# Kernel optimization log

Hardware: AMD Instinct MI355X
Metric: run time of the kernel (lower is better)

## Reference

```python
import jax, jax.numpy as jnp
import numpy as np

EMBED_DIM = 768
N_HEADS = 12
HEAD_DIM = EMBED_DIM // N_HEADS
B, T = 2, 4096


def setup_inputs() -> dict:
    key = jax.random.key(0)
    k1, k2, k3, k4, k5 = jax.random.split(key, 5)
    s = 1.0 / np.sqrt(EMBED_DIM)
    return {
        "x": jax.random.normal(k1, (B, T, EMBED_DIM), dtype=jnp.float32),
        "Wqkv": jax.random.normal(k2, (EMBED_DIM, 3 * EMBED_DIM), dtype=jnp.float32) * s,
        "bqkv": jnp.zeros((3 * EMBED_DIM,), dtype=jnp.float32),
        "Wproj": jax.random.normal(k3, (EMBED_DIM, EMBED_DIM), dtype=jnp.float32) * s,
        "bproj": jnp.zeros((EMBED_DIM,), dtype=jnp.float32),
    }


def reference(x, Wqkv, bqkv, Wproj, bproj):
    Bz, Tz, C = x.shape
    qkv = x @ Wqkv + bqkv                         # [B,T,3C]
    q, k, v = jnp.split(qkv, 3, axis=2)
    # [B,T,H,D] -> [B,H,T,D]
    def heads(t):
        return t.reshape(Bz, Tz, N_HEADS, HEAD_DIM).transpose(0, 2, 1, 3)
    q, k, v = heads(q), heads(k), heads(v)
    scale = 1.0 / np.sqrt(HEAD_DIM)
    att = jnp.einsum("bhqd,bhkd->bhqk", q, k) * scale   # [B,H,T,T]
    causal = jnp.tril(jnp.ones((Tz, Tz), dtype=bool))
    att = jnp.where(causal[None, None], att, -jnp.inf)
    att = jax.nn.softmax(att, axis=-1)
    y = jnp.einsum("bhqk,bhkd->bhqd", att, v)            # [B,H,T,D]
    y = y.transpose(0, 2, 1, 3).reshape(Bz, Tz, C)
    return y @ Wproj + bproj
```

## Files before the change

### kernel.cpp

```cpp
#include <hip/hip_runtime.h>
#include <math.h>
#include <stdint.h>

typedef __attribute__((ext_vector_type(8))) short bf16x8;
typedef __attribute__((ext_vector_type(4))) float f32x4;

__device__ __forceinline__ unsigned short f2bf(float f) {
    union { float f; unsigned u; } v; v.f = f;
    return (unsigned short)((v.u + 0x7fffu + ((v.u >> 16) & 1u)) >> 16);
}

__device__ __forceinline__ void gld_lds16(const void* g, void* l) {
    __builtin_amdgcn_global_load_lds(
        (const __attribute__((address_space(1))) unsigned*)(uintptr_t)g,
        (__attribute__((address_space(3))) unsigned*)(uintptr_t)l, 16, 0, 0);
}

__global__ void k_convert(const float* __restrict__ in, unsigned short* __restrict__ out, int n4) {
    int i = blockIdx.x * blockDim.x + threadIdx.x;
    if (i >= n4) return;
    float4 f = ((const float4*)in)[i];
    ushort4 o;
    o.x = f2bf(f.x); o.y = f2bf(f.y); o.z = f2bf(f.z); o.w = f2bf(f.w);
    ((ushort4*)out)[i] = o;
}

__global__ void k_transpose(const float* __restrict__ in, unsigned short* __restrict__ out, int R, int C) {
    __shared__ float tile[32][33];
    int c0 = blockIdx.x * 32, r0 = blockIdx.y * 32;
    int tx = threadIdx.x, ty = threadIdx.y;
#pragma unroll
    for (int i = 0; i < 4; ++i)
        tile[ty + i * 8][tx] = in[(size_t)(r0 + ty + i * 8) * C + c0 + tx];
    __syncthreads();
#pragma unroll
    for (int i = 0; i < 4; ++i)
        out[(size_t)(c0 + ty + i * 8) * R + r0 + tx] = f2bf(tile[tx][ty + i * 8]);
}

#define LDT 32

__device__ __forceinline__ void gemm_core(
    const unsigned short* __restrict__ A, const unsigned short* __restrict__ Bt,
    int K, unsigned short* As, unsigned short* Bs, f32x4 (&acc)[4][4])
{
    const int tid  = threadIdx.x;
    const int lane = tid & 63;
    const int w    = tid >> 6;
    const int wm   = (w >> 1) * 64, wn = (w & 1) * 64;
    const int l15  = lane & 15, quad = lane >> 4;
    const int m0 = blockIdx.x * 128, n0 = blockIdx.y * 128;

    const f32x4 zero = {0.f, 0.f, 0.f, 0.f};
#pragma unroll
    for (int i = 0; i < 4; ++i)
#pragma unroll
        for (int j = 0; j < 4; ++j) acc[i][j] = zero;

    const int r0 = tid >> 2, p8 = (tid & 3) * 8;
    const unsigned short* Ag0 = A  + (size_t)(m0 + r0) * K + p8;
    const unsigned short* Ag1 = A  + (size_t)(m0 + r0 + 64) * K + p8;
    const unsigned short* Bg0 = Bt + (size_t)(n0 + r0) * K + p8;
    const unsigned short* Bg1 = Bt + (size_t)(n0 + r0 + 64) * K + p8;
    unsigned short* lA0 = As + r0 * LDT + p8;
    unsigned short* lA1 = lA0 + 64 * LDT;
    unsigned short* lB0 = Bs + r0 * LDT + p8;
    unsigned short* lB1 = lB0 + 64 * LDT;

    const int nk = K >> 5;
    for (int kt = 0; kt < nk; ++kt) {
        __syncthreads();
        gld_lds16(Ag0, lA0);
        gld_lds16(Ag1, lA1);
        gld_lds16(Bg0, lB0);
        gld_lds16(Bg1, lB1);
        Ag0 += 32; Ag1 += 32; Bg0 += 32; Bg1 += 32;
        __syncthreads();
        bf16x8 af[4], bfr[4];
#pragma unroll
        for (int mi = 0; mi < 4; ++mi)
            af[mi] = *(const bf16x8*)&As[(wm + mi * 16 + l15) * LDT + quad * 8];
#pragma unroll
        for (int nj = 0; nj < 4; ++nj)
            bfr[nj] = *(const bf16x8*)&Bs[(wn + nj * 16 + l15) * LDT + quad * 8];
#pragma unroll
        for (int mi = 0; mi < 4; ++mi)
#pragma unroll
            for (int nj = 0; nj < 4; ++nj)
                acc[mi][nj] = __builtin_amdgcn_mfma_f32_16x16x32_bf16(af[mi], bfr[nj], acc[mi][nj], 0, 0, 0);
    }
}

__global__ __launch_bounds__(256) void k_gemm_qkv(
    const unsigned short* __restrict__ A, const unsigned short* __restrict__ Bt,
    const float* __restrict__ bias,
    unsigned short* __restrict__ QL, unsigned short* __restrict__ KL,
    unsigned short* __restrict__ VL)
{
    __shared__ __align__(16) unsigned short As[128 * LDT];
    __shared__ __align__(16) unsigned short Bs[128 * LDT];
    f32x4 acc[4][4];
    gemm_core(A, Bt, 768, As, Bs, acc);

    const int tid = threadIdx.x, lane = tid & 63, w = tid >> 6;
    const int wm = (w >> 1) * 64, wn = (w & 1) * 64;
    const int l15 = lane & 15, quad = lane >> 4;
    const int m0 = blockIdx.x * 128, n0 = blockIdx.y * 128;
    const float cscale = 0.18033688011f;
#pragma unroll
    for (int nj = 0; nj < 4; ++nj) {
        int cg = n0 + wn + nj * 16 + l15;
        float bv = bias[cg];
        int which = cg / 768;
        int rem = cg - which * 768;
        int hd = rem >> 6, d = rem & 63;
        float sc = (which == 0) ? cscale : 1.0f;
#pragma unroll
        for (int mi = 0; mi < 4; ++mi) {
#pragma unroll
            for (int r = 0; r < 4; ++r) {
                int rg = m0 + wm + mi * 16 + quad * 4 + r;
                int b = rg >> 12, tk = rg & 4095;
                int bh = b * 12 + hd;
                unsigned short ob = f2bf((acc[mi][nj][r] + bv) * sc);
                if (which == 0) {
                    size_t idx = ((((size_t)bh * 128 + (tk >> 5)) * 2 + ((tk >> 4) & 1)) * 2 + (d >> 5)) * 512
                               + ((d >> 3) & 3) * 128 + (tk & 15) * 8 + (d & 7);
                    QL[idx] = ob;
                } else if (which == 1) {
                    size_t idx = ((((size_t)bh * 64 + (tk >> 6)) * 4 + ((tk >> 4) & 3)) * 2 + (d >> 5)) * 512
                               + ((d >> 3) & 3) * 128 + (tk & 15) * 8 + (d & 7);
                    KL[idx] = ob;
                } else {
                    int wi = tk & 63;
                    size_t idx = ((((size_t)bh * 64 + (tk >> 6)) * 4 + (d >> 4)) * 2 + (wi >> 5)) * 512
                               + ((wi >> 3) & 3) * 128 + (d & 15) * 8 + (wi & 7);
                    VL[idx] = ob;
                }
            }
        }
    }
}

__global__ __launch_bounds__(256) void k_gemm_proj(
    const unsigned short* __restrict__ A, const unsigned short* __restrict__ Bt,
    const float* __restrict__ bias, float* __restrict__ out)
{
    __shared__ __align__(16) unsigned short As[128 * LDT];
    __shared__ __align__(16) unsigned short Bs[128 * LDT];
    f32x4 acc[4][4];
    gemm_core(A, Bt, 768, As, Bs, acc);

    const int tid = threadIdx.x, lane = tid & 63, w = tid >> 6;
    const int wm = (w >> 1) * 64, wn = (w & 1) * 64;
    const int l15 = lane & 15, quad = lane >> 4;
    const int m0 = blockIdx.x * 128, n0 = blockIdx.y * 128;
#pragma unroll
    for (int nj = 0; nj < 4; ++nj) {
        int cg = n0 + wn + nj * 16 + l15;
        float bv = bias[cg];
#pragma unroll
        for (int mi = 0; mi < 4; ++mi)
#pragma unroll
            for (int r = 0; r < 4; ++r) {
                int rg = m0 + wm + mi * 16 + quad * 4 + r;
                out[(size_t)rg * 768 + cg] = acc[mi][nj][r] + bv;
            }
    }
}

#define LDP 68

__global__ __launch_bounds__(128) void k_attn(
    const unsigned short* __restrict__ QL, const unsigned short* __restrict__ KL,
    const unsigned short* __restrict__ VL, unsigned short* __restrict__ Y)
{
    __shared__ __align__(16) char smem[17408];
    unsigned short* Ps = (unsigned short*)smem;
    float* Cb = (float*)smem;

    const int tid = threadIdx.x, lane = tid & 63;
    const int w = __builtin_amdgcn_readfirstlane(tid >> 6);
    const int l15 = lane & 15, quad = lane >> 4;
    const int id = blockIdx.x;
    const int bh = id % 24;
    const int qi = 127 - id / 24;
    const int q0 = qi * 32;
    const int nkt = qi / 2 + 1;
    const int lo = (nkt * w) >> 1, hi = (nkt * (w + 1)) >> 1;
    unsigned short* Pw = Ps + w * 2 * 32 * LDP;

    const int pw_off = l15 * LDP + quad * 4;
    const int pr_off = l15 * LDP + quad * 8;

    const unsigned short* Qb = QL + (((size_t)bh * 128 + qi) * 4) * 512 + lane * 8;
    const unsigned short* kp = KL + ((size_t)bh * 64 + lo) * 4096 + lane * 8;
    const unsigned short* vp = VL + ((size_t)bh * 64 + lo) * 4096 + lane * 8;

    bf16x8 qt[2][2];
#pragma unroll
    for (int m = 0; m < 2; ++m)
#pragma unroll
        for (int h = 0; h < 2; ++h)
            qt[m][h] = *(const bf16x8*)(Qb + (m * 2 + h) * 512);

    const f32x4 zero = {0.f, 0.f, 0.f, 0.f};
    f32x4 O[2][4], lac[2];
#pragma unroll
    for (int m = 0; m < 2; ++m) {
        lac[m] = zero;
#pragma unroll
        for (int dj = 0; dj < 4; ++dj) O[m][dj] = zero;
    }

    const short ONE = (short)0x3F80;
    const bf16x8 onesf = {ONE, ONE, ONE, ONE, ONE, ONE, ONE, ONE};

    if (lo < hi) {
        bf16x8 ka[4][2], vf[4][2];
#pragma unroll
        for (int i = 0; i < 4; ++i)
#pragma unroll
            for (int h = 0; h < 2; ++h)
                ka[i][h] = *(const bf16x8*)(kp + (i * 2 + h) * 512);
#pragma unroll
        for (int dj = 0; dj < 4; ++dj)
#pragma unroll
            for (int h = 0; h < 2; ++h)
                vf[dj][h] = *(const bf16x8*)(vp + (dj * 2 + h) * 512);

        {
            f32x4 st[2][4];
#pragma unroll
            for (int i = 0; i < 4; ++i)
#pragma unroll
                for (int m = 0; m < 2; ++m) {
                    f32x4 z = __builtin_amdgcn_mfma_f32_16x16x32_bf16(ka[i][0], qt[m][0], zero, 0, 0, 0);
                    st[m][i] = __builtin_amdgcn_mfma_f32_16x16x32_bf16(ka[i][1], qt[m][1], z, 0, 0, 0);
                }
            if (lo == nkt - 1) {
                const int kb = lo * 64;
#pragma unroll
                for (int m = 0; m < 2; ++m)
#pragma unroll
                    for (int i = 0; i < 4; ++i)
#pragma unroll
                        for (int r = 0; r < 4; ++r)
                            if (kb + i * 16 + quad * 4 + r > q0 + m * 16 + l15)
                                st[m][i][r] = -INFINITY;
            }
#pragma unroll
            for (int m = 0; m < 2; ++m)
#pragma unroll
                for (int i = 0; i < 4; ++i) {
                    unsigned e0 = __float_as_uint(__builtin_amdgcn_exp2f(st[m][i][0])) + 0x8000u;
                    unsigned e1 = __float_as_uint(__builtin_amdgcn_exp2f(st[m][i][1])) + 0x8000u;
                    unsigned e2 = __float_as_uint(__builtin_amdgcn_exp2f(st[m][i][2])) + 0x8000u;
                    unsigned e3 = __float_as_uint(__builtin_amdgcn_exp2f(st[m][i][3])) + 0x8000u;
                    uint2 pk;
                    pk.x = __builtin_amdgcn_perm(e1, e0, 0x07060302);
                    pk.y = __builtin_amdgcn_perm(e3, e2, 0x07060302);
                    *(uint2*)(Pw + pw_off + m * 16 * LDP + i * 16) = pk;
                }
        }

        for (int kt = lo; kt < hi; ++kt) {
            unsigned short* bc = Pw + ((kt - lo) & 1) * 32 * LDP;
            unsigned short* bn = Pw + (((kt - lo) & 1) ^ 1) * 32 * LDP;
            const bool more = (kt + 1 < hi);

            bf16x8 pa[2][2];
#pragma unroll
            for (int m = 0; m < 2; ++m) {
                pa[m][0] = *(const bf16x8*)(bc + pr_off + m * 16 * LDP);
                pa[m][1] = *(const bf16x8*)(bc + pr_off + m * 16 * LDP + 32);
            }

            if (more) {
                kp += 4096;
#pragma unroll
                for (int i = 0; i < 4; ++i)
#pragma unroll
                    for (int h = 0; h < 2; ++h)
                        ka[i][h] = *(const bf16x8*)(kp + (i * 2 + h) * 512);
            }

            __builtin_amdgcn_s_setprio(1);
#pragma unroll
            for (int m = 0; m < 2; ++m) {
                f32x4 z = __builtin_amdgcn_mfma_f32_16x16x32_bf16(pa[m][0], onesf, lac[m], 0, 0, 0);
                lac[m] = __builtin_amdgcn_mfma_f32_16x16x32_bf16(pa[m][1], onesf, z, 0, 0, 0);
            }
#pragma unroll
            for (int dj = 0; dj < 4; ++dj)
#pragma unroll
                for (int m = 0; m < 2; ++m) {
                    f32x4 z = __builtin_amdgcn_mfma_f32_16x16x32_bf16(pa[m][0], vf[dj][0], O[m][dj], 0, 0, 0);
                    O[m][dj] = __builtin_amdgcn_mfma_f32_16x16x32_bf16(pa[m][1], vf[dj][1], z, 0, 0, 0);
                }
            __builtin_amdgcn_s_setprio(0);

            if (more) {
                vp += 4096;
#pragma unroll
                for (int dj = 0; dj < 4; ++dj)
#pragma unroll
                    for (int h = 0; h < 2; ++h)
                        vf[dj][h] = *(const bf16x8*)(vp + (dj * 2 + h) * 512);

                __builtin_amdgcn_s_setprio(1);
                f32x4 st[2][4];
#pragma unroll
                for (int i = 0; i < 4; ++i)
#pragma unroll
                    for (int m = 0; m < 2; ++m) {
                        f32x4 z = __builtin_amdgcn_mfma_f32_16x16x32_bf16(ka[i][0], qt[m][0], zero, 0, 0, 0);
                        st[m][i] = __builtin_amdgcn_mfma_f32_16x16x32_bf16(ka[i][1], qt[m][1], z, 0, 0, 0);
                    }
                __builtin_amdgcn_s_setprio(0);
                if (kt + 1 == nkt - 1) {
                    const int kb = (kt + 1) * 64;
#pragma unroll
                    for (int m = 0; m < 2; ++m)
#pragma unroll
                        for (int i = 0; i < 4; ++i)
#pragma unroll
                            for (int r = 0; r < 4; ++r)
                                if (kb + i * 16 + quad * 4 + r > q0 + m * 16 + l15)
                                    st[m][i][r] = -INFINITY;
                }
#pragma unroll
                for (int m = 0; m < 2; ++m)
#pragma unroll
                    for (int i = 0; i < 4; ++i) {
                        unsigned e0 = __float_as_uint(__builtin_amdgcn_exp2f(st[m][i][0])) + 0x8000u;
                        unsigned e1 = __float_as_uint(__builtin_amdgcn_exp2f(st[m][i][1])) + 0x8000u;
                        unsigned e2 = __float_as_uint(__builtin_amdgcn_exp2f(st[m][i][2])) + 0x8000u;
                        unsigned e3 = __float_as_uint(__builtin_amdgcn_exp2f(st[m][i][3])) + 0x8000u;
                        uint2 pk;
                        pk.x = __builtin_amdgcn_perm(e1, e0, 0x07060302);
                        pk.y = __builtin_amdgcn_perm(e3, e2, 0x07060302);
                        *(uint2*)(bn + pw_off + m * 16 * LDP + i * 16) = pk;
                    }
            }
        }
    }

    __syncthreads();
    if (w == 1) {
#pragma unroll
        for (int m = 0; m < 2; ++m) {
#pragma unroll
            for (int dj = 0; dj < 4; ++dj)
                *(f32x4*)&Cb[(m * 4 + dj) * 256 + lane * 4] = O[m][dj];
            *(f32x4*)&Cb[2048 + m * 256 + lane * 4] = lac[m];
        }
    }
    __syncthreads();
    if (w == 0) {
#pragma unroll
        for (int m = 0; m < 2; ++m) {
#pragma unroll
            for (int dj = 0; dj < 4; ++dj)
                O[m][dj] += *(const f32x4*)&Cb[(m * 4 + dj) * 256 + lane * 4];
            lac[m] += *(const f32x4*)&Cb[2048 + m * 256 + lane * 4];
        }
        const int b = bh / 12, hd = bh % 12;
#pragma unroll
        for (int m = 0; m < 2; ++m)
#pragma unroll
            for (int r = 0; r < 4; ++r) {
                float inv = 1.0f / lac[m][r];
                int t = q0 + 16 * m + quad * 4 + r;
                size_t base = ((size_t)(b * 4096 + t)) * 768 + hd * 64;
#pragma unroll
                for (int dj = 0; dj < 4; ++dj)
                    Y[base + dj * 16 + l15] = f2bf(O[m][dj][r] * inv);
            }
    }
}

extern "C" void kernel_launch(void* const* d_in, const int* in_sizes, int n_in,
                              void* d_out, int out_size, void* d_ws, size_t ws_size,
                              hipStream_t stream) {
    (void)in_sizes; (void)n_in; (void)out_size; (void)ws_size;
    const float* x     = (const float*)d_in[0];
    const float* Wqkv  = (const float*)d_in[1];
    const float* bqkv  = (const float*)d_in[2];
    const float* Wproj = (const float*)d_in[3];
    const float* bproj = (const float*)d_in[4];
    float* out = (float*)d_out;

    char* ws = (char*)d_ws;
    size_t off = 0;
    auto alloc = [&](size_t bytes) -> void* {
        void* p = ws + off;
        off += (bytes + 255) & ~(size_t)255;
        return p;
    };
    unsigned short* xb     = (unsigned short*)alloc((size_t)8192 * 768 * 2);
    unsigned short* WqkvT  = (unsigned short*)alloc((size_t)2304 * 768 * 2);
    unsigned short* WprojT = (unsigned short*)alloc((size_t)768 * 768 * 2);
    unsigned short* QLb    = (unsigned short*)alloc((size_t)24 * 4096 * 64 * 2);
    unsigned short* KLb    = (unsigned short*)alloc((size_t)24 * 4096 * 64 * 2);
    unsigned short* VLb    = (unsigned short*)alloc((size_t)24 * 4096 * 64 * 2);
    unsigned short* Yb     = (unsigned short*)alloc((size_t)8192 * 768 * 2);

    k_convert<<<6144, 256, 0, stream>>>(x, xb, 8192 * 768 / 4);
    dim3 tb(32, 8);
    k_transpose<<<dim3(72, 24), tb, 0, stream>>>(Wqkv, WqkvT, 768, 2304);
    k_transpose<<<dim3(24, 24), tb, 0, stream>>>(Wproj, WprojT, 768, 768);
    k_gemm_qkv<<<dim3(64, 18), 256, 0, stream>>>(xb, WqkvT, bqkv, QLb, KLb, VLb);
    k_attn<<<dim3(3072), 128, 0, stream>>>(QLb, KLb, VLb, Yb);
    k_gemm_proj<<<dim3(64, 6), 256, 0, stream>>>(Yb, WprojT, bproj, out);
}
```

Measured before the change: 251.3 us.

## Pair short and long causal query tiles per block to balance attention work

Each attention block now handles two query tiles, a short one from the start of the sequence and its mirror from the end, which halves the grid. Wave 0 computes the short tile in full, writes it out, then takes a share of the long tile's key range. Wave 1 takes the rest of the long tile, and the two partial results are combined through LDS. This is meant to even out per-block work under the causal mask and cut tail imbalance, at the cost of fewer blocks and more serialized work per wave.

Result: slower. 264.0 us (+5.0%).

```diff
diff --git a/kernel.cpp b/kernel.cpp
--- a/kernel.cpp
+++ b/kernel.cpp
@@ -171,65 +171,114 @@
 
 #define LDP 68
 
-__global__ __launch_bounds__(128) void k_attn(
-    const unsigned short* __restrict__ QL, const unsigned short* __restrict__ KL,
-    const unsigned short* __restrict__ VL, unsigned short* __restrict__ Y)
-{
-    __shared__ __align__(16) char smem[17408];
-    unsigned short* Ps = (unsigned short*)smem;
-    float* Cb = (float*)smem;
-
-    const int tid = threadIdx.x, lane = tid & 63;
-    const int w = __builtin_amdgcn_readfirstlane(tid >> 6);
-    const int l15 = lane & 15, quad = lane >> 4;
-    const int id = blockIdx.x;
-    const int bh = id % 24;
-    const int qi = 127 - id / 24;
-    const int q0 = qi * 32;
-    const int nkt = qi / 2 + 1;
-    const int lo = (nkt * w) >> 1, hi = (nkt * (w + 1)) >> 1;
-    unsigned short* Pw = Ps + w * 2 * 32 * LDP;
-
-    const int pw_off = l15 * LDP + quad * 4;
-    const int pr_off = l15 * LDP + quad * 8;
-
-    const unsigned short* Qb = QL + (((size_t)bh * 128 + qi) * 4) * 512 + lane * 8;
-    const unsigned short* kp = KL + ((size_t)bh * 64 + lo) * 4096 + lane * 8;
-    const unsigned short* vp = VL + ((size_t)bh * 64 + lo) * 4096 + lane * 8;
-
-    bf16x8 qt[2][2];
-#pragma unroll
-    for (int m = 0; m < 2; ++m)
-#pragma unroll
-        for (int h = 0; h < 2; ++h)
-            qt[m][h] = *(const bf16x8*)(Qb + (m * 2 + h) * 512);
-
+__device__ __forceinline__ void attn_phase(
+    const unsigned short* __restrict__ Kbase,
+    const unsigned short* __restrict__ Vbase,
+    const bf16x8 (&qt)[2][2],
+    int t0, int t1, int ktd, int q0,
+    int l15, int quad,
+    unsigned short* Pw, int pw_off, int pr_off,
+    f32x4 (&O)[2][4], f32x4 (&lac)[2])
+{
     const f32x4 zero = {0.f, 0.f, 0.f, 0.f};
-    f32x4 O[2][4], lac[2];
-#pragma unroll
-    for (int m = 0; m < 2; ++m) {
-        lac[m] = zero;
-#pragma unroll
-        for (int dj = 0; dj < 4; ++dj) O[m][dj] = zero;
-    }
-
     const short ONE = (short)0x3F80;
     const bf16x8 onesf = {ONE, ONE, ONE, ONE, ONE, ONE, ONE, ONE};
 
-    if (lo < hi) {
-        bf16x8 ka[4][2], vf[4][2];
+    const unsigned short* kp = Kbase + (size_t)t0 * 4096;
+    const unsigned short* vp = Vbase + (size_t)t0 * 4096;
+
+    bf16x8 ka[4][2], vf[4][2];
+#pragma unroll
+    for (int i = 0; i < 4; ++i)
+#pragma unroll
+        for (int h = 0; h < 2; ++h)
+            ka[i][h] = *(const bf16x8*)(kp + (i * 2 + h) * 512);
+#pragma unroll
+    for (int dj = 0; dj < 4; ++dj)
+#pragma unroll
+        for (int h = 0; h < 2; ++h)
+            vf[dj][h] = *(const bf16x8*)(vp + (dj * 2 + h) * 512);
+
+    {
+        f32x4 st[2][4];
 #pragma unroll
         for (int i = 0; i < 4; ++i)
 #pragma unroll
-            for (int h = 0; h < 2; ++h)
-                ka[i][h] = *(const bf16x8*)(kp + (i * 2 + h) * 512);
+            for (int m = 0; m < 2; ++m) {
+                f32x4 z = __builtin_amdgcn_mfma_f32_16x16x32_bf16(ka[i][0], qt[m][0], zero, 0, 0, 0);
+                st[m][i] = __builtin_amdgcn_mfma_f32_16x16x32_bf16(ka[i][1], qt[m][1], z, 0, 0, 0);
+            }
+        if (t0 == ktd) {
+            const int kb = t0 * 64;
+#pragma unroll
+            for (int m = 0; m < 2; ++m)
+#pragma unroll
+                for (int i = 0; i < 4; ++i)
+#pragma unroll
+                    for (int r = 0; r < 4; ++r)
+                        if (kb + i * 16 + quad * 4 + r > q0 + m * 16 + l15)
+                            st[m][i][r] = -INFINITY;
+        }
+#pragma unroll
+        for (int m = 0; m < 2; ++m)
+#pragma unroll
+            for (int i = 0; i < 4; ++i) {
+                unsigned e0 = __float_as_uint(__builtin_amdgcn_exp2f(st[m][i][0])) + 0x8000u;
+                unsigned e1 = __float_as_uint(__builtin_amdgcn_exp2f(st[m][i][1])) + 0x8000u;
+                unsigned e2 = __float_as_uint(__builtin_amdgcn_exp2f(st[m][i][2])) + 0x8000u;
+                unsigned e3 = __float_as_uint(__builtin_amdgcn_exp2f(st[m][i][3])) + 0x8000u;
+                uint2 pk;
+                pk.x = __builtin_amdgcn_perm(e1, e0, 0x07060302);
+                pk.y = __builtin_amdgcn_perm(e3, e2, 0x07060302);
+                *(uint2*)(Pw + pw_off + m * 16 * LDP + i * 16) = pk;
+            }
+    }
+
+    for (int kt = t0; kt < t1; ++kt) {
+        unsigned short* bc = Pw + ((kt - t0) & 1) * 32 * LDP;
+        unsigned short* bn = Pw + (((kt - t0) & 1) ^ 1) * 32 * LDP;
+        const bool more = (kt + 1 < t1);
+
+        bf16x8 pa[2][2];
+#pragma unroll
+        for (int m = 0; m < 2; ++m) {
+            pa[m][0] = *(const bf16x8*)(bc + pr_off + m * 16 * LDP);
+            pa[m][1] = *(const bf16x8*)(bc + pr_off + m * 16 * LDP + 32);
+        }
+
+        if (more) {
+            kp += 4096;
+#pragma unroll
+            for (int i = 0; i < 4; ++i)
+#pragma unroll
+                for (int h = 0; h < 2; ++h)
+                    ka[i][h] = *(const bf16x8*)(kp + (i * 2 + h) * 512);
+        }
+
+        __builtin_amdgcn_s_setprio(1);
+#pragma unroll
+        for (int m = 0; m < 2; ++m) {
+            f32x4 z = __builtin_amdgcn_mfma_f32_16x16x32_bf16(pa[m][0], onesf, lac[m], 0, 0, 0);
+            lac[m] = __builtin_amdgcn_mfma_f32_16x16x32_bf16(pa[m][1], onesf, z, 0, 0, 0);
+        }
 #pragma unroll
         for (int dj = 0; dj < 4; ++dj)
 #pragma unroll
-            for (int h = 0; h < 2; ++h)
-                vf[dj][h] = *(const bf16x8*)(vp + (dj * 2 + h) * 512);
-
-        {
+            for (int m = 0; m < 2; ++m) {
+                f32x4 y = __builtin_amdgcn_mfma_f32_16x16x32_bf16(pa[m][0], vf[dj][0], O[m][dj], 0, 0, 0);
+                O[m][dj] = __builtin_amdgcn_mfma_f32_16x16x32_bf16(pa[m][1], vf[dj][1], y, 0, 0, 0);
+            }
+        __builtin_amdgcn_s_setprio(0);
+
+        if (more) {
+            vp += 4096;
+#pragma unroll
+            for (int dj = 0; dj < 4; ++dj)
+#pragma unroll
+                for (int h = 0; h < 2; ++h)
+                    vf[dj][h] = *(const bf16x8*)(vp + (dj * 2 + h) * 512);
+
+            __builtin_amdgcn_s_setprio(1);
             f32x4 st[2][4];
 #pragma unroll
             for (int i = 0; i < 4; ++i)
@@ -238,8 +287,9 @@
                     f32x4 z = __builtin_amdgcn_mfma_f32_16x16x32_bf16(ka[i][0], qt[m][0], zero, 0, 0, 0);
                     st[m][i] = __builtin_amdgcn_mfma_f32_16x16x32_bf16(ka[i][1], qt[m][1], z, 0, 0, 0);
                 }
-            if (lo == nkt - 1) {
-                const int kb = lo * 64;
+            __builtin_amdgcn_s_setprio(0);
+            if (kt + 1 == ktd) {
+                const int kb = (kt + 1) * 64;
 #pragma unroll
                 for (int m = 0; m < 2; ++m)
 #pragma unroll
@@ -260,94 +310,117 @@
                     uint2 pk;
                     pk.x = __builtin_amdgcn_perm(e1, e0, 0x07060302);
                     pk.y = __builtin_amdgcn_perm(e3, e2, 0x07060302);
-                    *(uint2*)(Pw + pw_off + m * 16 * LDP + i * 16) = pk;
+                    *(uint2*)(bn + pw_off + m * 16 * LDP + i * 16) = pk;
                 }
         }
-
-        for (int kt = lo; kt < hi; ++kt) {
-            unsigned short* bc = Pw + ((kt - lo) & 1) * 32 * LDP;
-            unsigned short* bn = Pw + (((kt - lo) & 1) ^ 1) * 32 * LDP;
-            const bool more = (kt + 1 < hi);
-
-            bf16x8 pa[2][2];
-#pragma unroll
-            for (int m = 0; m < 2; ++m) {
-                pa[m][0] = *(const bf16x8*)(bc + pr_off + m * 16 * LDP);
-                pa[m][1] = *(const bf16x8*)(bc + pr_off + m * 16 * LDP + 32);
-            }
-
-            if (more) {
-                kp += 4096;
-#pragma unroll
-                for (int i = 0; i < 4; ++i)
-#pragma unroll
-                    for (int h = 0; h < 2; ++h)
-                        ka[i][h] = *(const bf16x8*)(kp + (i * 2 + h) * 512);
-            }
-
-            __builtin_amdgcn_s_setprio(1);
-#pragma unroll
-            for (int m = 0; m < 2; ++m) {
-                f32x4 z = __builtin_amdgcn_mfma_f32_16x16x32_bf16(pa[m][0], onesf, lac[m], 0, 0, 0);
-                lac[m] = __builtin_amdgcn_mfma_f32_16x16x32_bf16(pa[m][1], onesf, z, 0, 0, 0);
-            }
+    }
+}
+
+__device__ __forceinline__ void attn_writeout(
+    const f32x4 (&O)[2][4], const f32x4 (&lac)[2],
+    int q0, int b, int hd, int quad, int l15, unsigned short* __restrict__ Y)
+{
+#pragma unroll
+    for (int m = 0; m < 2; ++m)
+#pragma unroll
+        for (int r = 0; r < 4; ++r) {
+            float inv = 1.0f / lac[m][r];
+            int t = q0 + 16 * m + quad * 4 + r;
+            size_t base = ((size_t)(b * 4096 + t)) * 768 + hd * 64;
 #pragma unroll
             for (int dj = 0; dj < 4; ++dj)
-#pragma unroll
-                for (int m = 0; m < 2; ++m) {
-                    f32x4 z = __builtin_amdgcn_mfma_f32_16x16x32_bf16(pa[m][0], vf[dj][0], O[m][dj], 0, 0, 0);
-                    O[m][dj] = __builtin_amdgcn_mfma_f32_16x16x32_bf16(pa[m][1], vf[dj][1], z, 0, 0, 0);
-                }
-            __builtin_amdgcn_s_setprio(0);
-
-            if (more) {
-                vp += 4096;
-#pragma unroll
-                for (int dj = 0; dj < 4; ++dj)
-#pragma unroll
-                    for (int h = 0; h < 2; ++h)
-                        vf[dj][h] = *(const bf16x8*)(vp + (dj * 2 + h) * 512);
-
-                __builtin_amdgcn_s_setprio(1);
-                f32x4 st[2][4];
-#pragma unroll
-                for (int i = 0; i < 4; ++i)
-#pragma unroll
-                    for (int m = 0; m < 2; ++m) {
-                        f32x4 z = __builtin_amdgcn_mfma_f32_16x16x32_bf16(ka[i][0], qt[m][0], zero, 0, 0, 0);
-                        st[m][i] = __builtin_amdgcn_mfma_f32_16x16x32_bf16(ka[i][1], qt[m][1], z, 0, 0, 0);
-                    }
-                __builtin_amdgcn_s_setprio(0);
-                if (kt + 1 == nkt - 1) {
-                    const int kb = (kt + 1) * 64;
-#pragma unroll
-                    for (int m = 0; m < 2; ++m)
-#pragma unroll
-                        for (int i = 0; i < 4; ++i)
-#pragma unroll
-                            for (int r = 0; r < 4; ++r)
-                                if (kb + i * 16 + quad * 4 + r > q0 + m * 16 + l15)
-                                    st[m][i][r] = -INFINITY;
-                }
-#pragma unroll
-                for (int m = 0; m < 2; ++m)
-#pragma unroll
-                    for (int i = 0; i < 4; ++i) {
-                        unsigned e0 = __float_as_uint(__builtin_amdgcn_exp2f(st[m][i][0])) + 0x8000u;
-                        unsigned e1 = __float_as_uint(__builtin_amdgcn_exp2f(st[m][i][1])) + 0x8000u;
-                        unsigned e2 = __float_as_uint(__builtin_amdgcn_exp2f(st[m][i][2])) + 0x8000u;
-                        unsigned e3 = __float_as_uint(__builtin_amdgcn_exp2f(st[m][i][3])) + 0x8000u;
-                        uint2 pk;
-                        pk.x = __builtin_amdgcn_perm(e1, e0, 0x07060302);
-                        pk.y = __builtin_amdgcn_perm(e3, e2, 0x07060302);
-                        *(uint2*)(bn + pw_off + m * 16 * LDP + i * 16) = pk;
-                    }
-            }
-        }
+                Y[base + dj * 16 + l15] = f2bf(O[m][dj][r] * inv);
+        }
+}
+
+__global__ __launch_bounds__(128) void k_attn(
+    const unsigned short* __restrict__ QL, const unsigned short* __restrict__ KL,
+    const unsigned short* __restrict__ VL, unsigned short* __restrict__ Y)
+{
+    __shared__ __align__(16) char smem[17408];
+    unsigned short* Ps = (unsigned short*)smem;
+    float* Cb = (float*)smem;
+
+    const int tid = threadIdx.x, lane = tid & 63;
+    const int w = __builtin_amdgcn_readfirstlane(tid >> 6);
+    const int l15 = lane & 15, quad = lane >> 4;
+    const int id = blockIdx.x;
+    const int bh = id % 24;
+    const int p  = id / 24;
+    const int qs = p, ql = 127 - p;
+    const int s  = p / 2 + 1;
+    const int nl = ql / 2 + 1;
+    const int cA = (nl - s) / 2;
+    unsigned short* Pw = Ps + w * 2 * 32 * LDP;
+
+    const int pw_off = l15 * LDP + quad * 4;
+    const int pr_off = l15 * LDP + quad * 8;
+
+    const unsigned short* Kbase = KL + ((size_t)bh * 64) * 4096 + lane * 8;
+    const unsigned short* Vbase = VL + ((size_t)bh * 64) * 4096 + lane * 8;
+    const int b = bh / 12, hd = bh % 12;
+
+    const f32x4 zero = {0.f, 0.f, 0.f, 0.f};
+    f32x4 O[2][4], lac[2];
+    bf16x8 qt[2][2];
+
+    if (w == 0) {
+        {
+            const unsigned short* Qb = QL + (((size_t)bh * 128 + qs) * 4) * 512 + lane * 8;
+#pragma unroll
+            for (int m = 0; m < 2; ++m)
+#pragma unroll
+                for (int h = 0; h < 2; ++h)
+                    qt[m][h] = *(const bf16x8*)(Qb + (m * 2 + h) * 512);
+        }
+#pragma unroll
+        for (int m = 0; m < 2; ++m) {
+            lac[m] = zero;
+#pragma unroll
+            for (int dj = 0; dj < 4; ++dj) O[m][dj] = zero;
+        }
+        attn_phase(Kbase, Vbase, qt, 0, s, s - 1, qs * 32, l15, quad,
+                   Pw, pw_off, pr_off, O, lac);
+        attn_writeout(O, lac, qs * 32, b, hd, quad, l15, Y);
+
+        {
+            const unsigned short* Qb = QL + (((size_t)bh * 128 + ql) * 4) * 512 + lane * 8;
+#pragma unroll
+            for (int m = 0; m < 2; ++m)
+#pragma unroll
+                for (int h = 0; h < 2; ++h)
+                    qt[m][h] = *(const bf16x8*)(Qb + (m * 2 + h) * 512);
+        }
+#pragma unroll
+        for (int m = 0; m < 2; ++m) {
+            lac[m] = zero;
+#pragma unroll
+            for (int dj = 0; dj < 4; ++dj) O[m][dj] = zero;
+        }
+        if (cA > 0)
+            attn_phase(Kbase, Vbase, qt, 0, cA, -1, ql * 32, l15, quad,
+                       Pw, pw_off, pr_off, O, lac);
+    } else {
+        {
+            const unsigned short* Qb = QL + (((size_t)bh * 128 + ql) * 4) * 512 + lane * 8;
+#pragma unroll
+            for (int m = 0; m < 2; ++m)
+#pragma unroll
+                for (int h = 0; h < 2; ++h)
+                    qt[m][h] = *(const bf16x8*)(Qb + (m * 2 + h) * 512);
+        }
+#pragma unroll
+        for (int m = 0; m < 2; ++m) {
+            lac[m] = zero;
+#pragma unroll
+            for (int dj = 0; dj < 4; ++dj) O[m][dj] = zero;
+        }
+        attn_phase(Kbase, Vbase, qt, cA, nl, nl - 1, ql * 32, l15, quad,
+                   Pw, pw_off, pr_off, O, lac);
     }
 
     __syncthreads();
-    if (w == 1) {
+    if (w == 0) {
 #pragma unroll
         for (int m = 0; m < 2; ++m) {
 #pragma unroll
@@ -357,7 +430,7 @@
         }
     }
     __syncthreads();
-    if (w == 0) {
+    if (w == 1) {
 #pragma unroll
         for (int m = 0; m < 2; ++m) {
 #pragma unroll
@@ -365,18 +438,7 @@
                 O[m][dj] += *(const f32x4*)&Cb[(m * 4 + dj) * 256 + lane * 4];
             lac[m] += *(const f32x4*)&Cb[2048 + m * 256 + lane * 4];
         }
-        const int b = bh / 12, hd = bh % 12;
-#pragma unroll
-        for (int m = 0; m < 2; ++m)
-#pragma unroll
-            for (int r = 0; r < 4; ++r) {
-                float inv = 1.0f / lac[m][r];
-                int t = q0 + 16 * m + quad * 4 + r;
-                size_t base = ((size_t)(b * 4096 + t)) * 768 + hd * 64;
-#pragma unroll
-                for (int dj = 0; dj < 4; ++dj)
-                    Y[base + dj * 16 + l15] = f2bf(O[m][dj][r] * inv);
-            }
+        attn_writeout(O, lac, ql * 32, b, hd, quad, l15, Y);
     }
 }
 
@@ -411,6 +473,6 @@
     k_transpose<<<dim3(72, 24), tb, 0, stream>>>(Wqkv, WqkvT, 768, 2304);
     k_transpose<<<dim3(24, 24), tb, 0, stream>>>(Wproj, WprojT, 768, 768);
     k_gemm_qkv<<<dim3(64, 18), 256, 0, stream>>>(xb, WqkvT, bqkv, QLb, KLb, VLb);
-    k_attn<<<dim3(3072), 128, 0, stream>>>(QLb, KLb, VLb, Yb);
+    k_attn<<<dim3(1536), 128, 0, stream>>>(QLb, KLb, VLb, Yb);
     k_gemm_proj<<<dim3(64, 6), 256, 0, stream>>>(Yb, WprojT, bproj, out);
 }
```
